# Performance work log

Measured on AMD Instinct MI355X. Metric: run time of the kernel, lower is better.

## Reference

```python
import jax, jax.numpy as jnp
import numpy as np

E, K, IN_DIM, OUT_DIM = 100000, 16, 128, 128


def _linear_init(key, out_d, in_d):
    kw, kb = jax.random.split(key)
    bound = 1.0 / np.sqrt(in_d)
    W = jax.random.uniform(kw, (out_d, in_d), minval=-bound, maxval=bound, dtype=jnp.float32)
    b = jax.random.uniform(kb, (out_d,), minval=-bound, maxval=bound, dtype=jnp.float32)
    return W, b


def setup_inputs() -> dict:
    key = jax.random.key(0)
    k_feat, k_adj, k1, k2, k3, k4 = jax.random.split(key, 6)
    edge_features = jax.random.normal(k_feat, (E, IN_DIM), dtype=jnp.float32)
    edge_adjacency = jax.random.randint(k_adj, (E, K), 0, E, dtype=jnp.int64)
    mW1, mb1 = _linear_init(k1, OUT_DIM, 2 * IN_DIM)
    mW2, mb2 = _linear_init(k2, OUT_DIM, OUT_DIM)
    uW1, ub1 = _linear_init(k3, OUT_DIM, IN_DIM + OUT_DIM)
    uW2, ub2 = _linear_init(k4, OUT_DIM, OUT_DIM)
    return {"edge_features": edge_features, "edge_adjacency": edge_adjacency,
            "mW1": mW1, "mb1": mb1, "mW2": mW2, "mb2": mb2,
            "uW1": uW1, "ub1": ub1, "uW2": ub2 * 0 + ub2 if False else uW1 * 0 + uW1 if False else uW1, "ub1_": ub1} if False else {
            "edge_features": edge_features, "edge_adjacency": edge_adjacency,
            "mW1": mW1, "mb1": mb1, "mW2": mW2, "mb2": mb2,
            "uW1": uW1, "ub1": ub1, "uW2": uW2, "ub2": ub2}


def reference(edge_features, edge_adjacency, mW1, mb1, mW2, mb2, uW1, ub1, uW2, ub2):
    D = edge_features.shape[1]
    # message_net first Linear on concat([feat_i, feat_j]) split into two halves
    # to avoid materializing the [E, K, 2D] concat tensor.
    Wi, Wj = mW1[:, :D], mW1[:, D:]                      # each [O, D]
    self_part = edge_features @ Wi.T                     # [E, O]
    nbr_feat = edge_features[edge_adjacency]             # [E, K, D] gather
    h = jax.nn.relu(self_part[:, None, :] + jnp.einsum('ekd,od->eko', nbr_feat, Wj) + mb1)
    msg = jnp.einsum('eko,po->ekp', h, mW2) + mb2        # [E, K, O]
    msg = msg.mean(axis=1)                               # mean over neighbors -> [E, O]
    # update_net on concat([feat_i, msg_i]), split likewise
    Ui, Um = uW1[:, :D], uW1[:, D:]
    u = jax.nn.relu(edge_features @ Ui.T + msg @ Um.T + ub1)
    return u @ uW2.T + ub2                               # [E, O]
```

## Files before the change

### kernel.cpp

```cpp
#include <hip/hip_runtime.h>
#include <hip/hip_bf16.h>

#define NE 100000
#define NK 16
#define ND 128
#define NTILES 6250
#define NSUP 3125

typedef __bf16 bf16_t;
typedef bf16_t bf16x8 __attribute__((ext_vector_type(8)));
typedef bf16_t bf16x4 __attribute__((ext_vector_type(4)));
typedef float f32x4 __attribute__((ext_vector_type(4)));
typedef float f32x2 __attribute__((ext_vector_type(2)));
typedef unsigned u32x2 __attribute__((ext_vector_type(2)));
typedef unsigned short u16;
typedef unsigned char u8;

__device__ __forceinline__ u16 f2bf(float f) {
  bf16_t h = (bf16_t)f;
  return __builtin_bit_cast(u16, h);
}

__device__ __forceinline__ void soft_barrier() {
  asm volatile("s_waitcnt lgkmcnt(0)" ::: "memory");
  __builtin_amdgcn_s_barrier();
}

__device__ __forceinline__ void unpack_s(unsigned w0, unsigned w1,
                                         f32x4& sA, f32x4& sB) {
  const f32x2 a0 = __builtin_amdgcn_cvt_pk_f32_fp8(w0, false);
  const f32x2 a1 = __builtin_amdgcn_cvt_pk_f32_fp8(w0, true);
  const f32x2 a2 = __builtin_amdgcn_cvt_pk_f32_fp8(w1, false);
  const f32x2 a3 = __builtin_amdgcn_cvt_pk_f32_fp8(w1, true);
  sA[0] = a0[0]; sA[1] = a0[1]; sA[2] = a1[0]; sA[3] = a1[1];
  sB[0] = a2[0]; sB[1] = a2[1]; sB[2] = a3[0]; sB[3] = a3[1];
}

__device__ __forceinline__ void acc8(f32x4& hA, f32x4& hB,
                                     const f32x4 sA, const f32x4 sB,
                                     const u32x2 zw) {
  const f32x2 z0 = __builtin_amdgcn_cvt_pk_f32_fp8(zw[0], false);
  const f32x2 z1 = __builtin_amdgcn_cvt_pk_f32_fp8(zw[0], true);
  const f32x2 z2 = __builtin_amdgcn_cvt_pk_f32_fp8(zw[1], false);
  const f32x2 z3 = __builtin_amdgcn_cvt_pk_f32_fp8(zw[1], true);
  f32x4 vA = sA, vB = sB;
  vA[0] += z0[0]; vA[1] += z0[1]; vA[2] += z1[0]; vA[3] += z1[1];
  vB[0] += z2[0]; vB[1] += z2[1]; vB[2] += z3[0]; vB[3] += z3[1];
#pragma unroll
  for (int i = 0; i < 4; ++i) {
    vA[i] = fmaxf(vA[i], 0.f);
    vB[i] = fmaxf(vB[i], 0.f);
  }
  hA += vA;
  hB += vB;
}

__global__ void k_prep(const float* __restrict__ mW1, const float* __restrict__ uW1,
                       const float* __restrict__ uW2, const float* __restrict__ mW2,
                       const float* __restrict__ ub1, const float* __restrict__ mb2,
                       u16* __restrict__ Wi_b, u16* __restrict__ Wj_b,
                       u16* __restrict__ Ui_b, u16* __restrict__ Wp_b,
                       u16* __restrict__ W2_b, float* __restrict__ bp)
{
  const int o = blockIdx.x, t = threadIdx.x;
  Wi_b[o * ND + t] = f2bf(mW1[o * 256 + t]);
  Wj_b[o * ND + t] = f2bf(mW1[o * 256 + 128 + t]);
  Ui_b[o * ND + t] = f2bf(uW1[o * 256 + t]);
  W2_b[o * ND + t] = f2bf(uW2[o * ND + t]);
  float acc = 0.f;
  for (int p = 0; p < 128; ++p)
    acc += uW1[o * 256 + 128 + p] * mW2[p * 128 + t];
  Wp_b[o * ND + t] = f2bf(acc);
  if (t == 0) {
    float b = ub1[o];
    for (int p = 0; p < 128; ++p) b += uW1[o * 256 + 128 + p] * mb2[p];
    bp[o] = b;
  }
}

__global__ __launch_bounds__(512) void k1_szt(
    const float* __restrict__ X, const u16* __restrict__ Wi_b,
    const u16* __restrict__ Wj_b, const u16* __restrict__ Ui_b,
    const float* __restrict__ mb1, const float* __restrict__ bp,
    u8* __restrict__ Sf8, u8* __restrict__ Zf8, u16* __restrict__ Tp)
{
  __shared__ u16 xt[2][16 * ND];
  __shared__ u8  eS[2][16 * ND];
  __shared__ u8  eZ[2][16 * ND];
  __shared__ u16 eT[2][16 * ND];
  const int tid = threadIdx.x, wid = tid >> 6, lane = tid & 63;
  const int r = lane & 15, q = lane >> 4;

  bf16x8 wiF[4], wjF[4], uiF[4];
  f32x4 mbF, bpF;
  {
    const int row = wid * 16 + r;
#pragma unroll
    for (int kk = 0; kk < 4; ++kk) {
      wiF[kk] = *(const bf16x8*)(Wi_b + row * ND + kk * 32 + q * 8);
      wjF[kk] = *(const bf16x8*)(Wj_b + row * ND + kk * 32 + q * 8);
      uiF[kk] = *(const bf16x8*)(Ui_b + row * ND + kk * 32 + q * 8);
    }
    mbF = *(const f32x4*)(mb1 + wid * 16 + q * 4);
    bpF = *(const f32x4*)(bp  + wid * 16 + q * 4);
  }

  const int rs = tid >> 5, cs = tid & 31;
  const int stb = rs * 256 + ((((cs >> 1) ^ (rs & 15)) << 4) | ((cs & 1) << 3));
  const int ewb = r * 256 + ((((wid * 2 + (q >> 1)) ^ (r & 15)) << 4) | ((q & 1) << 3));
  const int ezb = r * 128 + (((wid ^ (r & 7)) << 4) | (q * 4));
  const int erow = tid >> 5, c8 = tid & 31;
  const int erb = erow * 256 + ((((c8 >> 1) ^ (erow & 15)) << 4) | ((c8 & 1) << 3));
  const int zrb = erow * 128 + ((((c8 >> 2) ^ (erow & 7)) << 4) | ((c8 & 3) << 2));

  const long stride = gridDim.x;
  long t = blockIdx.x;
  if (t >= NTILES) return;

  f32x4 xr;
  auto gload = [&](long tt) {
    xr = *(const f32x4*)(X + (tt * 16 + rs) * ND + cs * 4);
  };
  auto stage = [&](int bb) {
    bf16x4 b;
#pragma unroll
    for (int i = 0; i < 4; ++i) b[i] = (bf16_t)xr[i];
    *(bf16x4*)((char*)xt[bb] + stb) = b;
  };

  gload(t);
  stage(0);
  {
    const long t1 = t + stride;
    if (t1 < NTILES) gload(t1);
  }
  soft_barrier();
  int b = 0;

  for (; t < NTILES; t += stride) {
    const long tn = t + stride, tn2 = tn + stride;

    bf16x8 xf[4];
#pragma unroll
    for (int kk = 0; kk < 4; ++kk)
      xf[kk] = *(const bf16x8*)((const char*)xt[b] +
               r * 256 + (((kk * 4 + q) ^ (r & 15)) << 4));

    if (tn < NTILES) stage(b ^ 1);
    if (tn2 < NTILES) gload(tn2);

    f32x4 aS = {0.f, 0.f, 0.f, 0.f};
    f32x4 aZ = {0.f, 0.f, 0.f, 0.f};
    f32x4 aT = {0.f, 0.f, 0.f, 0.f};
#pragma unroll
    for (int kk = 0; kk < 4; ++kk) {
      aS = __builtin_amdgcn_mfma_f32_16x16x32_bf16(wiF[kk], xf[kk], aS, 0, 0, 0);
      aZ = __builtin_amdgcn_mfma_f32_16x16x32_bf16(wjF[kk], xf[kk], aZ, 0, 0, 0);
      aT = __builtin_amdgcn_mfma_f32_16x16x32_bf16(uiF[kk], xf[kk], aT, 0, 0, 0);
    }

    bf16x4 pT;
#pragma unroll
    for (int i = 0; i < 4; ++i) pT[i] = (bf16_t)(aT[i] + bpF[i]);
    unsigned spk = 0, zpk = 0;
    spk = __builtin_amdgcn_cvt_pk_fp8_f32(aS[0] + mbF[0], aS[1] + mbF[1], spk, false);
    spk = __builtin_amdgcn_cvt_pk_fp8_f32(aS[2] + mbF[2], aS[3] + mbF[3], spk, true);
    zpk = __builtin_amdgcn_cvt_pk_fp8_f32(aZ[0], aZ[1], zpk, false);
    zpk = __builtin_amdgcn_cvt_pk_fp8_f32(aZ[2], aZ[3], zpk, true);
    *(unsigned*)((char*)eS[b] + ezb) = spk;
    *(unsigned*)((char*)eZ[b] + ezb) = zpk;
    *(bf16x4*)((char*)eT[b] + ewb) = pT;

    soft_barrier();

    {
      const long e = t * 16 + erow;
      const unsigned vS = *(const unsigned*)((const char*)eS[b] + zrb);
      const unsigned vZ = *(const unsigned*)((const char*)eZ[b] + zrb);
      const bf16x4 vT = *(const bf16x4*)((const char*)eT[b] + erb);
      *(unsigned*)(Sf8 + e * ND + c8 * 4) = vS;
      *(unsigned*)(Zf8 + e * ND + c8 * 4) = vZ;
      *(bf16x4*)(Tp + t * 2048 + erow * 128 + c8 * 4) = vT;
    }
    b ^= 1;
  }
}

__global__ __launch_bounds__(512) void k23_fused(
    const u8* __restrict__ Zf8, const u8* __restrict__ Sf8,
    const int* __restrict__ adj, const u16* __restrict__ Tp,
    const u16* __restrict__ Wp_b, const u16* __restrict__ W2_b,
    const float* __restrict__ ub2, float* __restrict__ out)
{
  __shared__ u16 ht[32 * ND];
  __shared__ u16 tt[32 * ND];
  __shared__ u16 ut[32 * ND];
  const int tid = threadIdx.x, wid = tid >> 6, lane = tid & 63;
  const int r = lane & 15, q = lane >> 4;
  const int ew = wid * 4 + q;
  const int c0 = r * 8;
  const long s = blockIdx.x;

  f32x4 haccA = {0.f, 0.f, 0.f, 0.f}, haccB = {0.f, 0.f, 0.f, 0.f};
  bf16x8 trC;
  {
    const int myidxC = adj[(s * 32 + ew) * NK + r];
    const unsigned* sp = (const unsigned*)(Sf8 + (s * 32 + ew) * ND + c0);
    const unsigned sw0 = sp[0], sw1 = sp[1];
    const int trow = tid >> 4, tch = tid & 15;
    trC = *(const bf16x8*)(Tp + s * 4096 + trow * 128 + tch * 8);

    f32x4 sA, sB;
    unpack_s(sw0, sw1, sA, sB);
    u32x2 zb[8];
#pragma unroll
    for (int k = 0; k < 8; ++k) {
      const int n = __shfl(myidxC, (lane & 48) + k);
      zb[k] = *(const u32x2*)(Zf8 + (long)n * ND + c0);
    }
#pragma unroll
    for (int k = 0; k < 8; ++k) acc8(haccA, haccB, sA, sB, zb[k]);
#pragma unroll
    for (int k = 0; k < 8; ++k) {
      const int n = __shfl(myidxC, (lane & 48) + 8 + k);
      zb[k] = *(const u32x2*)(Zf8 + (long)n * ND + c0);
    }
#pragma unroll
    for (int k = 0; k < 8; ++k) acc8(haccA, haccB, sA, sB, zb[k]);
  }

  bf16x8 wpF[4], w2F[4];
  f32x4 ubF;
  {
    const int row = wid * 16 + r;
#pragma unroll
    for (int kk = 0; kk < 4; ++kk) {
      wpF[kk] = *(const bf16x8*)(Wp_b + row * ND + kk * 32 + q * 8);
      w2F[kk] = *(const bf16x8*)(W2_b + row * ND + kk * 32 + q * 8);
    }
    ubF = *(const f32x4*)(ub2 + wid * 16 + q * 4);
  }

  const int hwb = ew * 256 + ((r ^ (ew & 15)) << 4);
  const int trow = tid >> 4, tch = tid & 15;
  const int twb = trow * 256 + ((tch ^ (trow & 15)) << 4);
  const int uwb0 = (((wid * 2 + (q >> 1)) ^ r) << 4) | ((q & 1) << 3);
  {
    bf16x8 hv;
#pragma unroll
    for (int i = 0; i < 4; ++i) {
      hv[i]     = (bf16_t)(haccA[i] * 0.0625f);
      hv[i + 4] = (bf16_t)(haccB[i] * 0.0625f);
    }
    *(bf16x8*)((char*)ht + hwb) = hv;
    *(bf16x8*)((char*)tt + twb) = trC;
  }

  soft_barrier();

#pragma unroll
  for (int t2 = 0; t2 < 2; ++t2) {
    const int rowb = (t2 * 16 + r) * 256;
    bf16x8 hf[4];
#pragma unroll
    for (int kk = 0; kk < 4; ++kk)
      hf[kk] = *(const bf16x8*)((const char*)ht + rowb + (((kk * 4 + q) ^ r) << 4));
    f32x4 acc;
    {
      const bf16x4 tv = *(const bf16x4*)((const char*)tt + rowb + uwb0);
#pragma unroll
      for (int i = 0; i < 4; ++i) acc[i] = (float)tv[i];
    }
#pragma unroll
    for (int kk = 0; kk < 4; ++kk)
      acc = __builtin_amdgcn_mfma_f32_16x16x32_bf16(wpF[kk], hf[kk], acc, 0, 0, 0);
    bf16x4 u;
#pragma unroll
    for (int i = 0; i < 4; ++i) u[i] = (bf16_t)fmaxf(acc[i], 0.f);
    *(bf16x4*)((char*)ut + rowb + uwb0) = u;
  }

  soft_barrier();

#pragma unroll
  for (int t2 = 0; t2 < 2; ++t2) {
    const int rowb = (t2 * 16 + r) * 256;
    bf16x8 uf[4];
#pragma unroll
    for (int kk = 0; kk < 4; ++kk)
      uf[kk] = *(const bf16x8*)((const char*)ut + rowb + (((kk * 4 + q) ^ r) << 4));
    f32x4 o = {0.f, 0.f, 0.f, 0.f};
#pragma unroll
    for (int kk = 0; kk < 4; ++kk)
      o = __builtin_amdgcn_mfma_f32_16x16x32_bf16(w2F[kk], uf[kk], o, 0, 0, 0);
#pragma unroll
    for (int i = 0; i < 4; ++i) o[i] += ubF[i];
    *(f32x4*)(out + (s * 32 + t2 * 16 + r) * ND + wid * 16 + q * 4) = o;
  }
}

extern "C" void kernel_launch(void* const* d_in, const int* in_sizes, int n_in,
                              void* d_out, int out_size, void* d_ws, size_t ws_size,
                              hipStream_t stream)
{
  (void)in_sizes; (void)n_in; (void)out_size; (void)ws_size;
  const float* X   = (const float*)d_in[0];
  const int*   adj = (const int*)d_in[1];
  const float* mW1 = (const float*)d_in[2];
  const float* mb1 = (const float*)d_in[3];
  const float* mW2 = (const float*)d_in[4];
  const float* mb2 = (const float*)d_in[5];
  const float* uW1 = (const float*)d_in[6];
  const float* ub1 = (const float*)d_in[7];
  const float* uW2 = (const float*)d_in[8];
  const float* ub2 = (const float*)d_in[9];
  float* out = (float*)d_out;

  u8* ws8  = (u8*)d_ws;
  u8* Sf8  = ws8;
  u8* Zf8  = Sf8 + (size_t)NE * ND;
  u16* Tp  = (u16*)(Zf8 + (size_t)NE * ND);
  u16* Wi_b = Tp + (size_t)NE * ND;
  u16* Wj_b = Wi_b + 128 * 128;
  u16* Ui_b = Wj_b + 128 * 128;
  u16* Wp_b = Ui_b + 128 * 128;
  u16* W2_b = Wp_b + 128 * 128;
  float* bp = (float*)(W2_b + 128 * 128);

  k_prep<<<128, 128, 0, stream>>>(mW1, uW1, uW2, mW2, ub1, mb2,
                                  Wi_b, Wj_b, Ui_b, Wp_b, W2_b, bp);

  k1_szt<<<1024, 512, 0, stream>>>(X, Wi_b, Wj_b, Ui_b, mb1, bp, Sf8, Zf8, Tp);

  k23_fused<<<NSUP, 512, 0, stream>>>(Zf8, Sf8, adj, Tp, Wp_b, W2_b, ub2, out);
}
```

Before: 89.51 us.

## Shrink fused gather/MLP kernel to 16-edge tiles with 256 threads

The fused message/update kernel now handles 16 edges per block with 4 waves instead of 32 edges with 8 waves, launching twice as many blocks. Each wave now owns two output column tiles, loading weight fragments for both and reusing a single set of LDS row fragments. All 16 neighbor loads are issued before any accumulation to raise memory-level parallelism. The cost is more per-block weight fetching from cache, more registers per thread, and less reuse of weights across edges.

Result: slower. 103.3 us (+15.4%).

```diff
diff --git a/kernel.cpp b/kernel.cpp
--- a/kernel.cpp
+++ b/kernel.cpp
@@ -5,7 +5,6 @@
 #define NK 16
 #define ND 128
 #define NTILES 6250
-#define NSUP 3125
 
 typedef __bf16 bf16_t;
 typedef bf16_t bf16x8 __attribute__((ext_vector_type(8)));
@@ -186,65 +185,45 @@
   }
 }
 
-__global__ __launch_bounds__(512) void k23_fused(
+__global__ __launch_bounds__(256) void k23_os(
     const u8* __restrict__ Zf8, const u8* __restrict__ Sf8,
     const int* __restrict__ adj, const u16* __restrict__ Tp,
     const u16* __restrict__ Wp_b, const u16* __restrict__ W2_b,
     const float* __restrict__ ub2, float* __restrict__ out)
 {
-  __shared__ u16 ht[32 * ND];
-  __shared__ u16 tt[32 * ND];
-  __shared__ u16 ut[32 * ND];
+  __shared__ u16 ht[16 * ND];
+  __shared__ u16 tt[16 * ND];
+  __shared__ u16 ut[16 * ND];
   const int tid = threadIdx.x, wid = tid >> 6, lane = tid & 63;
   const int r = lane & 15, q = lane >> 4;
   const int ew = wid * 4 + q;
   const int c0 = r * 8;
-  const long s = blockIdx.x;
+  const long t = blockIdx.x;
 
   f32x4 haccA = {0.f, 0.f, 0.f, 0.f}, haccB = {0.f, 0.f, 0.f, 0.f};
   bf16x8 trC;
   {
-    const int myidxC = adj[(s * 32 + ew) * NK + r];
-    const unsigned* sp = (const unsigned*)(Sf8 + (s * 32 + ew) * ND + c0);
+    const int myidxC = adj[(t * 16 + ew) * NK + r];
+    const unsigned* sp = (const unsigned*)(Sf8 + (t * 16 + ew) * ND + c0);
     const unsigned sw0 = sp[0], sw1 = sp[1];
     const int trow = tid >> 4, tch = tid & 15;
-    trC = *(const bf16x8*)(Tp + s * 4096 + trow * 128 + tch * 8);
-
+    trC = *(const bf16x8*)(Tp + t * 2048 + trow * 128 + tch * 8);
+
+    u32x2 zb[16];
+#pragma unroll
+    for (int k = 0; k < 16; ++k) {
+      const int n = __shfl(myidxC, (lane & 48) + k);
+      zb[k] = *(const u32x2*)(Zf8 + (long)n * ND + c0);
+    }
     f32x4 sA, sB;
     unpack_s(sw0, sw1, sA, sB);
-    u32x2 zb[8];
-#pragma unroll
-    for (int k = 0; k < 8; ++k) {
-      const int n = __shfl(myidxC, (lane & 48) + k);
-      zb[k] = *(const u32x2*)(Zf8 + (long)n * ND + c0);
-    }
-#pragma unroll
-    for (int k = 0; k < 8; ++k) acc8(haccA, haccB, sA, sB, zb[k]);
-#pragma unroll
-    for (int k = 0; k < 8; ++k) {
-      const int n = __shfl(myidxC, (lane & 48) + 8 + k);
-      zb[k] = *(const u32x2*)(Zf8 + (long)n * ND + c0);
-    }
-#pragma unroll
-    for (int k = 0; k < 8; ++k) acc8(haccA, haccB, sA, sB, zb[k]);
-  }
-
-  bf16x8 wpF[4], w2F[4];
-  f32x4 ubF;
-  {
-    const int row = wid * 16 + r;
-#pragma unroll
-    for (int kk = 0; kk < 4; ++kk) {
-      wpF[kk] = *(const bf16x8*)(Wp_b + row * ND + kk * 32 + q * 8);
-      w2F[kk] = *(const bf16x8*)(W2_b + row * ND + kk * 32 + q * 8);
-    }
-    ubF = *(const f32x4*)(ub2 + wid * 16 + q * 4);
+#pragma unroll
+    for (int k = 0; k < 16; ++k) acc8(haccA, haccB, sA, sB, zb[k]);
   }
 
   const int hwb = ew * 256 + ((r ^ (ew & 15)) << 4);
   const int trow = tid >> 4, tch = tid & 15;
   const int twb = trow * 256 + ((tch ^ (trow & 15)) << 4);
-  const int uwb0 = (((wid * 2 + (q >> 1)) ^ r) << 4) | ((q & 1) << 3);
   {
     bf16x8 hv;
 #pragma unroll
@@ -256,46 +235,64 @@
     *(bf16x8*)((char*)tt + twb) = trC;
   }
 
+  bf16x8 wpF[2][4];
+  f32x4 ubF[2];
+#pragma unroll
+  for (int j = 0; j < 2; ++j) {
+    const int row = (2 * wid + j) * 16 + r;
+#pragma unroll
+    for (int kk = 0; kk < 4; ++kk)
+      wpF[j][kk] = *(const bf16x8*)(Wp_b + row * ND + kk * 32 + q * 8);
+    ubF[j] = *(const f32x4*)(ub2 + (2 * wid + j) * 16 + q * 4);
+  }
+
   soft_barrier();
 
-#pragma unroll
-  for (int t2 = 0; t2 < 2; ++t2) {
-    const int rowb = (t2 * 16 + r) * 256;
-    bf16x8 hf[4];
-#pragma unroll
-    for (int kk = 0; kk < 4; ++kk)
-      hf[kk] = *(const bf16x8*)((const char*)ht + rowb + (((kk * 4 + q) ^ r) << 4));
+  bf16x8 hf[4];
+#pragma unroll
+  for (int kk = 0; kk < 4; ++kk)
+    hf[kk] = *(const bf16x8*)((const char*)ht +
+             r * 256 + (((kk * 4 + q) ^ (r & 15)) << 4));
+#pragma unroll
+  for (int j = 0; j < 2; ++j) {
+    const int ct = 2 * wid + j;
+    const int cb = r * 256 + ((((ct * 2 + (q >> 1)) ^ (r & 15)) << 4) | ((q & 1) << 3));
     f32x4 acc;
     {
-      const bf16x4 tv = *(const bf16x4*)((const char*)tt + rowb + uwb0);
+      const bf16x4 tv = *(const bf16x4*)((const char*)tt + cb);
 #pragma unroll
       for (int i = 0; i < 4; ++i) acc[i] = (float)tv[i];
     }
 #pragma unroll
     for (int kk = 0; kk < 4; ++kk)
-      acc = __builtin_amdgcn_mfma_f32_16x16x32_bf16(wpF[kk], hf[kk], acc, 0, 0, 0);
+      acc = __builtin_amdgcn_mfma_f32_16x16x32_bf16(wpF[j][kk], hf[kk], acc, 0, 0, 0);
     bf16x4 u;
 #pragma unroll
     for (int i = 0; i < 4; ++i) u[i] = (bf16_t)fmaxf(acc[i], 0.f);
-    *(bf16x4*)((char*)ut + rowb + uwb0) = u;
+    *(bf16x4*)((char*)ut + cb) = u;
   }
 
   soft_barrier();
 
-#pragma unroll
-  for (int t2 = 0; t2 < 2; ++t2) {
-    const int rowb = (t2 * 16 + r) * 256;
-    bf16x8 uf[4];
-#pragma unroll
-    for (int kk = 0; kk < 4; ++kk)
-      uf[kk] = *(const bf16x8*)((const char*)ut + rowb + (((kk * 4 + q) ^ r) << 4));
+  bf16x8 uf[4];
+#pragma unroll
+  for (int kk = 0; kk < 4; ++kk)
+    uf[kk] = *(const bf16x8*)((const char*)ut +
+             r * 256 + (((kk * 4 + q) ^ (r & 15)) << 4));
+#pragma unroll
+  for (int j = 0; j < 2; ++j) {
+    const int ct = 2 * wid + j;
+    bf16x8 w2F[4];
+#pragma unroll
+    for (int kk = 0; kk < 4; ++kk)
+      w2F[kk] = *(const bf16x8*)(W2_b + (ct * 16 + r) * ND + kk * 32 + q * 8);
     f32x4 o = {0.f, 0.f, 0.f, 0.f};
 #pragma unroll
     for (int kk = 0; kk < 4; ++kk)
       o = __builtin_amdgcn_mfma_f32_16x16x32_bf16(w2F[kk], uf[kk], o, 0, 0, 0);
 #pragma unroll
-    for (int i = 0; i < 4; ++i) o[i] += ubF[i];
-    *(f32x4*)(out + (s * 32 + t2 * 16 + r) * ND + wid * 16 + q * 4) = o;
+    for (int i = 0; i < 4; ++i) o[i] += ubF[j][i];
+    *(f32x4*)(out + (t * 16 + r) * ND + ct * 16 + q * 4) = o;
   }
 }
 
@@ -332,5 +329,5 @@
 
   k1_szt<<<1024, 512, 0, stream>>>(X, Wi_b, Wj_b, Ui_b, mb1, bp, Sf8, Zf8, Tp);
 
-  k23_fused<<<NSUP, 512, 0, stream>>>(Zf8, Sf8, adj, Tp, Wp_b, W2_b, ub2, out);
-}
+  k23_os<<<NTILES, 256, 0, stream>>>(Zf8, Sf8, adj, Tp, Wp_b, W2_b, ub2, out);
+}
```
